# Kernel optimization log

Hardware: AMD Instinct MI355X
Metric: run time of the kernel (lower is better)

Reference implementation:

```python
import jax, jax.numpy as jnp
import numpy as np

# Module hyperparameters (from init_kwargs)
B, C, T, H, W = 2, 128, 4, 64, 64
NHEADS = 32
SH, SW = 4, 4          # scales: patch size in H and W
GROUPS = C // 4        # GroupNorm groups = dim // 4
EPS = 1e-5


def _rel_index(t_, h_, w_):
    """(N,N) int32 index into the (2T-1)*(2h-1)*(2w-1) relative-position table."""
    tt = np.arange(t_); yy = np.arange(h_); xx = np.arange(w_)
    coords = np.stack(np.meshgrid(tt, yy, xx, indexing='ij'), -1).reshape(-1, 3)  # (N,3)
    rel = coords[:, None, :] - coords[None, :, :]                                 # (N,N,3)
    rel = rel + np.array([t_ - 1, h_ - 1, w_ - 1])
    idx = (rel[..., 0] * (2 * h_ - 1) + rel[..., 1]) * (2 * w_ - 1) + rel[..., 2]
    return idx.astype(np.int32)


def setup_inputs() -> dict:
    key = jax.random.key(0)
    ks = jax.random.split(key, 6)
    h, w = H // SH, W // SW
    table_sz = (2 * T - 1) * (2 * h - 1) * (2 * w - 1)
    inp = {
        "x": jax.random.normal(ks[0], (B, C, T, H, W), jnp.float32),
        "Wq": jax.random.normal(ks[1], (C, C), jnp.float32) / np.sqrt(C).astype(np.float32),
        "Wk": jax.random.normal(ks[2], (C, C), jnp.float32) / np.sqrt(C).astype(np.float32),
        "Wv": jax.random.normal(ks[3], (C, C), jnp.float32) / np.sqrt(C).astype(np.float32),
        "gq_gamma": jnp.ones((C,), jnp.float32), "gq_beta": jnp.zeros((C,), jnp.float32),
        "gk_gamma": jnp.ones((C,), jnp.float32), "gk_beta": jnp.zeros((C,), jnp.float32),
        "gv_gamma": jnp.ones((C,), jnp.float32), "gv_beta": jnp.zeros((C,), jnp.float32),
        "rel_table": jax.random.normal(ks[4], (NHEADS, table_sz), jnp.float32) * 0.02,
        "rel_index": jnp.asarray(_rel_index(T, h, w)),
    }
    return inp


def _group_norm(z, gamma, beta, groups, eps=EPS):
    b, c = z.shape[:2]
    zg = z.reshape(b, groups, c // groups, *z.shape[2:])
    mu = zg.mean(axis=(2, 3, 4, 5), keepdims=True)
    var = jnp.mean(jnp.square(zg - mu), axis=(2, 3, 4, 5), keepdims=True)
    zg = (zg - mu) * jax.lax.rsqrt(var + eps)
    zn = zg.reshape(z.shape)
    return zn * gamma[None, :, None, None, None] + beta[None, :, None, None, None]


def reference(x, Wq, Wk, Wv, gq_gamma, gq_beta, gk_gamma, gk_beta,
              gv_gamma, gv_beta, rel_table, rel_index):
    b, c, t, hh, ww = x.shape
    h, w = hh // SH, ww // SW
    n = t * h * w           # patch tokens
    p = SH * SW             # pixels per patch
    d = c // NHEADS         # head dim

    # 1x1x1 projections (pointwise conv == channel matmul) + GroupNorm
    q = _group_norm(jnp.einsum('bcthw,oc->bothw', x, Wq), gq_gamma, gq_beta, GROUPS)
    k = _group_norm(jnp.einsum('bcthw,oc->bothw', x, Wk), gk_gamma, gk_beta, GROUPS)
    v = _group_norm(jnp.einsum('bcthw,oc->bothw', x, Wv), gv_gamma, gv_beta, GROUPS)

    def to_patches(z):  # (b,c,t,H,W) -> (b,heads,d,N,P)
        z = z.reshape(b, NHEADS, d, t, h, SH, w, SW)
        z = z.transpose(0, 1, 2, 3, 4, 6, 5, 7)
        return z.reshape(b, NHEADS, d, n, p)

    qp = to_patches(q).mean(-1)     # pooled patch queries (b,g,d,N)
    kp = to_patches(k).mean(-1)     # pooled patch keys    (b,g,d,N)
    vp = to_patches(v)              # full-res values      (b,g,d,N,P)

    scale = 1.0 / jnp.sqrt(jnp.float32(d))
    logits = jnp.einsum('bgdn,bgdm->bgnm', qp, kp) * scale
    logits = logits + rel_table[:, rel_index][None]   # relative position bias (1,g,N,N)
    attn = jax.nn.softmax(logits, axis=-1)

    out = jnp.einsum('bgnm,bgdmp->bgdnp', attn, vp)   # (b,g,d,N,P)
    out = out.reshape(b, NHEADS, d, t, h, w, SH, SW).transpose(0, 1, 2, 3, 4, 6, 5, 7)
    out = out.reshape(b, c, t, hh, ww)                # (B,C,T,H,W) after outer permute
    return out
```

## Files before the change

### kernel.cpp

```cpp
#include <hip/hip_runtime.h>
#include <hip/hip_bf16.h>

#define B_ 2
#define C_ 128
#define G_ 32
#define N_ 1024
#define S_ 16384
#define TABLE_ 6727
#define EPS_ 1e-5f
#define LOG2E_ 1.44269504f
#define PSTB_ 64

typedef __hip_bfloat16 bf16;
typedef __attribute__((ext_vector_type(8))) short short8;
typedef __attribute__((ext_vector_type(4))) float f32x4;

#if __has_builtin(__builtin_amdgcn_exp2f)
#define EXP2(x) __builtin_amdgcn_exp2f(x)
#else
#define EXP2(x) __expf((x) * 0.69314718056f)
#endif

__device__ __forceinline__ float bf2f(bf16 v) { return __bfloat162float(v); }
__device__ __forceinline__ float bits2f(unsigned u) { return __uint_as_float(u); }
__device__ __forceinline__ int dflag(const void* gq) {
  return (((const unsigned*)gq)[0] != 0x3F803F80u) ? 1 : 0;
}
__device__ __forceinline__ float ldcv(const void* p, int i, int fl) {
  return fl ? ((const float*)p)[i] : bf2f(((const bf16*)p)[i]);
}

__global__ __launch_bounds__(256) void proj_kernel(
    const void* __restrict__ x, const void* __restrict__ Wq,
    const void* __restrict__ Wk, const void* __restrict__ Wv,
    const void* __restrict__ gq,
    float* __restrict__ qpart, float* __restrict__ kpart,
    bf16* __restrict__ vpt, float* __restrict__ statsAcc)
{
  __shared__ bf16 xs[128 * 128];
  __shared__ bf16 vs[8192];
  const int tid = threadIdx.x, lane = tid & 63, w = tid >> 6;
  const int s0 = blockIdx.x * 128;
  const int oh = blockIdx.y;
  const int b  = blockIdx.z;
  const int fl = dflag(gq);

  {
    const int s_lo = tid & 15, cb = tid >> 4;
    const size_t gc = (size_t)b * C_ * S_ + (size_t)(cb * 8) * S_ + s0 + s_lo;
#pragma unroll
    for (int i = 0; i < 8; ++i) {
      const int s = i * 16 + s_lo;
      union { short8 v; bf16 h[8]; } u;
      if (fl) {
#pragma unroll
        for (int j = 0; j < 8; ++j)
          u.h[j] = (bf16)((const float*)x)[gc + i * 16 + (size_t)j * S_];
      } else {
#pragma unroll
        for (int j = 0; j < 8; ++j)
          u.h[j] = ((const bf16*)x)[gc + i * 16 + (size_t)j * S_];
      }
      *(short8*)&xs[s * 128 + ((cb ^ (s & 7)) << 3)] = u.v;
    }
  }

  const int ow = oh * 4 + w;
  const int quad = lane >> 4;
  const int om = ow * 16 + (lane & 15);
  const void* const Ws[3] = {Wq, Wk, Wv};
  short8 afr[3][4];
#pragma unroll
  for (int tt = 0; tt < 3; ++tt)
#pragma unroll
    for (int kk = 0; kk < 4; ++kk) {
      const int off = om * 128 + kk * 32 + quad * 8;
      if (fl) {
        const float* wp = (const float*)Ws[tt] + off;
        const float4 a = *(const float4*)wp, bb = *(const float4*)(wp + 4);
        union { short8 s; bf16 h[8]; } u;
        u.h[0] = (bf16)a.x;  u.h[1] = (bf16)a.y;  u.h[2] = (bf16)a.z;  u.h[3] = (bf16)a.w;
        u.h[4] = (bf16)bb.x; u.h[5] = (bf16)bb.y; u.h[6] = (bf16)bb.z; u.h[7] = (bf16)bb.w;
        afr[tt][kk] = u.s;
      } else {
        afr[tt][kk] = *(const short8*)((const bf16*)Ws[tt] + off);
      }
    }
  __syncthreads();

  float ssum[3] = {0.f, 0.f, 0.f}, ssq[3] = {0.f, 0.f, 0.f};
  float psq[4][4] = {}, psk[4][4] = {};
  const int sl = lane & 15;
#pragma unroll
  for (int st = 0; st < 8; ++st) {
    f32x4 acc[3] = {{0,0,0,0},{0,0,0,0},{0,0,0,0}};
    const int srow = st * 16 + sl;
#pragma unroll
    for (int kk = 0; kk < 4; ++kk) {
      const short8 bv = *(const short8*)
          &xs[srow * 128 + ((((kk << 2) | quad) ^ (sl & 7)) << 3)];
      acc[0] = __builtin_amdgcn_mfma_f32_16x16x32_bf16(afr[0][kk], bv, acc[0], 0, 0, 0);
      acc[1] = __builtin_amdgcn_mfma_f32_16x16x32_bf16(afr[1][kk], bv, acc[1], 0, 0, 0);
      acc[2] = __builtin_amdgcn_mfma_f32_16x16x32_bf16(afr[2][kk], bv, acc[2], 0, 0, 0);
    }
    const int pIdx = (st >> 2) * 4 + (sl & 3);
    const int xp = (st & 3) * 4 + (sl >> 2);
#pragma unroll
    for (int r = 0; r < 4; ++r) {
      const float vq = acc[0][r], vk = acc[1][r], vv = acc[2][r];
      ssum[0] += vq; ssq[0] += vq * vq;
      ssum[1] += vk; ssq[1] += vk * vk;
      ssum[2] += vv; ssq[2] += vv * vv;
      float aq = vq + __shfl_xor(vq, 1); aq += __shfl_xor(aq, 2);
      float ak = vk + __shfl_xor(vk, 1); ak += __shfl_xor(ak, 2);
      psq[r][st & 3] += aq;
      psk[r][st & 3] += ak;
      const int o_loc = w * 16 + quad * 4 + r;
      vs[(o_loc * 8 + pIdx) * 16 + xp] = (bf16)vv;
    }
  }

  {
    const int c = sl & 3, wxl = sl >> 2;
    const int t = s0 >> 12;
    const int yy0 = (s0 >> 6) & 63;
    const int hy = yy0 >> 2, rp = (yy0 >> 1) & 1;
    const int nbase = t * 256 + hy * 16;
    const size_t pb = ((size_t)(b * 2 + rp) * N_ + nbase) * C_ + ow * 16 + quad * 4 + c;
#pragma unroll
    for (int j = 0; j < 4; ++j) {
      float vq = psq[0][j];
      if (c == 1) vq = psq[1][j];
      if (c == 2) vq = psq[2][j];
      if (c == 3) vq = psq[3][j];
      float vk = psk[0][j];
      if (c == 1) vk = psk[1][j];
      if (c == 2) vk = psk[2][j];
      if (c == 3) vk = psk[3][j];
      qpart[pb + (size_t)(j * 4 + wxl) * C_] = vq;
      kpart[pb + (size_t)(j * 4 + wxl) * C_] = vk;
    }
  }

#pragma unroll
  for (int tt = 0; tt < 3; ++tt) {
#pragma unroll
    for (int off = 1; off < 16; off <<= 1) {
      ssum[tt] += __shfl_xor(ssum[tt], off);
      ssq[tt]  += __shfl_xor(ssq[tt], off);
    }
    if ((lane & 15) == 0) {
      const int grp = ow * 4 + quad;
      atomicAdd(&statsAcc[((tt * B_ + b) * G_ + grp) * 2 + 0], ssum[tt]);
      atomicAdd(&statsAcc[((tt * B_ + b) * G_ + grp) * 2 + 1], ssq[tt]);
    }
  }
  __syncthreads();

  const int rowp0 = (s0 >> 6) & 63;
  const int mIdx0 = (s0 >> 12) * 256 + (rowp0 >> 2) * 16;
  for (int cid = tid; cid < 1024; cid += 256) {
    const int half = cid & 1, run = cid >> 1;
    const int o_loc = run >> 3, pIdx = run & 7;
    const int o = oh * 64 + o_loc;
    const int gg = o >> 2, dd = o & 3;
    const int colv = dd * 16 + (rowp0 & 3) * 4 + pIdx;
    bf16* dst = vpt + ((size_t)(b * G_ + gg) * 64 + colv) * N_ + mIdx0 + half * 8;
    *(short8*)dst = *(const short8*)&vs[run * 16 + half * 8];
  }
}

__global__ __launch_bounds__(256) void pool_kernel(
    const float* __restrict__ qpart, const float* __restrict__ kpart,
    const void* __restrict__ gq, const void* __restrict__ bq,
    const void* __restrict__ gk, const void* __restrict__ bk,
    const float* __restrict__ statsAcc,
    bf16* __restrict__ qp2, bf16* __restrict__ kp2)
{
  const int fl = dflag(gq);
  const int idx = blockIdx.x * 256 + threadIdx.x;
  const int c = idx & 127, n = (idx >> 7) & 1023, b = idx >> 17;
  const int g = c >> 2, d = c & 3;
  const size_t p0 = ((size_t)(b * 2 + 0) * N_ + n) * C_ + c;
  const size_t p1 = ((size_t)(b * 2 + 1) * N_ + n) * C_ + c;
  const float sq = qpart[p0] + qpart[p1];
  const float sk = kpart[p0] + kpart[p1];
  const float* saq = statsAcc + ((0 * B_ + b) * G_ + g) * 2;
  const float* sak = statsAcc + ((1 * B_ + b) * G_ + g) * 2;
  const float muq = saq[0] * (1.f / 65536.f);
  const float rq = rsqrtf(saq[1] * (1.f / 65536.f) - muq * muq + EPS_);
  const float muk = sak[0] * (1.f / 65536.f);
  const float rk = rsqrtf(sak[1] * (1.f / 65536.f) - muk * muk + EPS_);
  const float qn = (sq * 0.0625f - muq) * rq * ldcv(gq, c, fl) + ldcv(bq, c, fl);
  const float kn = (sk * 0.0625f - muk) * rk * ldcv(gk, c, fl) + ldcv(bk, c, fl);
  const float qs = qn * (0.5f * LOG2E_);
  const bf16 qh = (bf16)qs; const bf16 ql = (bf16)(qs - bf2f(qh));
  const bf16 kh = (bf16)kn; const bf16 kl = (bf16)(kn - bf2f(kh));
  const size_t qb = ((size_t)(b * G_ + g) * N_ + n) * 8;
  qp2[qb + d] = qh; qp2[qb + 4 + d] = ql;
  kp2[qb + d] = kh; kp2[qb + 4 + d] = kl;
}

__global__ __launch_bounds__(256, 4) void attn_kernel(
    const bf16* __restrict__ qp2, const bf16* __restrict__ kp2,
    const bf16* __restrict__ vpt, const void* __restrict__ rt,
    const void* __restrict__ gq, const void* __restrict__ gv,
    const void* __restrict__ bv, const float* __restrict__ statsAcc,
    void* __restrict__ outv)
{
  const int g = blockIdx.y, b = blockIdx.z;
  const int tid = threadIdx.x, lane = tid & 63, w = tid >> 6;
  const int nw = blockIdx.x * 64;
  const int fl = dflag(gq);
  __shared__ __align__(16) char smem[16384 + 5024 + 8192];
  bf16* Vlds = (bf16*)smem;
  bf16* bldm = (bf16*)(smem + 16384);
  bf16* pldw = (bf16*)(smem + 16384 + 5024) + w * 16 * PSTB_;

  const int tn = nw >> 8, yb = (nw >> 4) & 15;
  for (int i = tid; i < 2508; i += 256) {
    const int row = i / 33, d = i - row * 33;
    if (d < 31) {
      const int tm = row / 19, dyi = row - tm * 19;
      const int dt = tn - tm + 3;
      const int dy = yb + dyi;
      bldm[row * 33 + d] = (bf16)(ldcv(rt, g * TABLE_ + (dt * 31 + dy) * 31 + d, fl) * LOG2E_);
    }
  }

  const int col = lane & 15, quad = lane >> 4;
  const size_t bg = (size_t)(b * G_ + g);
  short8 af = {0, 0, 0, 0, 0, 0, 0, 0};
  if (quad < 2) af = *(const short8*)(qp2 + (bg * N_ + nw + w * 16 + col) * 8);

  const short* kpb = (const short*)kp2 + bg * N_ * 8;
  const short* vpb = (const short*)vpt + bg * 64 * N_;
  const short onebits = (short)0x3F80;
  const short8 ones8 = {onebits, onebits, onebits, onebits,
                        onebits, onebits, onebits, onebits};
  f32x4 acco[4] = {{0,0,0,0},{0,0,0,0},{0,0,0,0},{0,0,0,0}};
  f32x4 accs = {0.f, 0.f, 0.f, 0.f};

  const int skb = tid & 15, snr = tid >> 4;

  ushort4 kv[4], kvn[4];
#pragma unroll
  for (int t = 0; t < 4; ++t)
    kv[t] = *(const ushort4*)(kpb + ((0 * 4 + t) * 16 + col) * 8 + (quad & 1) * 4);

  for (int tile = 0; tile < 8; ++tile) {
    __syncthreads();
    short8 st[4];
#pragma unroll
    for (int i = 0; i < 4; ++i)
      st[i] = *(const short8*)(vpb + (size_t)(i * 16 + snr) * N_ + tile * 128 + skb * 8);
#pragma unroll
    for (int i = 0; i < 4; ++i) {
      const int n = i * 16 + snr;
      *(short8*)&Vlds[n * 128 + ((skb ^ (n & 7)) << 3)] = st[i];
    }
    __syncthreads();

    for (int cl = 0; cl < 2; ++cl) {
      const int ch = tile * 2 + cl;
      if (ch < 15) {
#pragma unroll
        for (int t = 0; t < 4; ++t)
          kvn[t] = *(const ushort4*)(kpb + (((ch + 1) * 4 + t) * 16 + col) * 8 + (quad & 1) * 4);
      }
#pragma unroll
      for (int mt4 = 0; mt4 < 4; ++mt4) {
        const int mt = ch * 4 + mt4;
        const int tm = mt >> 4, ym = mt & 15;
        const short8 bf8 = {(short)kv[mt4].x, (short)kv[mt4].y, (short)kv[mt4].z, (short)kv[mt4].w,
                            (short)kv[mt4].x, (short)kv[mt4].y, (short)kv[mt4].z, (short)kv[mt4].w};
        f32x4 acc = {0.f, 0.f, 0.f, 0.f};
        acc = __builtin_amdgcn_mfma_f32_16x16x32_bf16(af, bf8, acc, 0, 0, 0);
        const int bbase = (tm * 19 + (w + 15 - ym)) * 33 + 15 + quad * 4 - col;
#pragma unroll
        for (int r = 0; r < 4; ++r) {
          const float e = EXP2(acc[r] + bf2f(bldm[bbase + r]));
          const int row = quad * 4 + r;
          pldw[row * PSTB_ + (((mt4 * 2 + (col >> 3)) ^ (row & 7)) << 3) + (col & 7)] = (bf16)e;
        }
      }
#pragma unroll
      for (int ks = 0; ks < 2; ++ks) {
        const short8 a2 = *(const short8*)&pldw[col * PSTB_ + (((ks * 4 + quad) ^ (col & 7)) << 3)];
        accs = __builtin_amdgcn_mfma_f32_16x16x32_bf16(a2, ones8, accs, 0, 0, 0);
#pragma unroll
        for (int cc = 0; cc < 4; ++cc) {
          const int n = cc * 16 + col;
          const int kb = cl * 8 + ks * 4 + quad;
          const short8 b2 = *(const short8*)&Vlds[n * 128 + ((kb ^ (n & 7)) << 3)];
          acco[cc] = __builtin_amdgcn_mfma_f32_16x16x32_bf16(a2, b2, acco[cc], 0, 0, 0);
        }
      }
      if (ch < 15) {
#pragma unroll
        for (int t = 0; t < 4; ++t) kv[t] = kvn[t];
      }
    }
  }

  __syncthreads();
  const float* sav = statsAcc + ((2 * B_ + b) * G_ + g) * 2;
  const float mu = sav[0] * (1.f / 65536.f);
  const float rs = rsqrtf(sav[1] * (1.f / 65536.f) - mu * mu + EPS_);
  const int sh = col >> 2, sw = col & 3;
  const size_t obase = (size_t)(b * C_ + g * 4) * S_ + tn * 4096 + (yb + w) * 256;
  if (!fl) {
    bf16* ost = (bf16*)(smem + w * 2048);
#pragma unroll
    for (int cc = 0; cc < 4; ++cc) {
      const int c = g * 4 + cc;
      const float alpha = rs * ldcv(gv, c, fl);
      const float beta = ldcv(bv, c, fl) - mu * alpha;
#pragma unroll
      for (int r = 0; r < 4; ++r) {
        const int xp = quad * 4 + r;
        ost[cc * 256 + sh * 64 + xp * 4 + sw] = (bf16)(alpha * (acco[cc][r] / accs[r]) + beta);
      }
    }
#pragma unroll
    for (int i = 0; i < 2; ++i) {
      const int e = (i * 64 + lane) * 8;
      const int cc = e >> 8, rem = e & 255;
      *(short8*)((bf16*)outv + obase + (size_t)cc * S_ + rem) = *(const short8*)&ost[e];
    }
  } else {
    float* ostf = (float*)smem + w * 1024;
#pragma unroll
    for (int cc = 0; cc < 4; ++cc) {
      const int c = g * 4 + cc;
      const float alpha = rs * ldcv(gv, c, fl);
      const float beta = ldcv(bv, c, fl) - mu * alpha;
#pragma unroll
      for (int r = 0; r < 4; ++r) {
        const int xp = quad * 4 + r;
        ostf[cc * 256 + sh * 64 + xp * 4 + sw] = alpha * (acco[cc][r] / accs[r]) + beta;
      }
    }
#pragma unroll
    for (int i = 0; i < 4; ++i) {
      const int e = (i * 64 + lane) * 4;
      const int cc = e >> 8, rem = e & 255;
      *(float4*)((float*)outv + obase + (size_t)cc * S_ + rem) = *(const float4*)&ostf[e];
    }
  }
}

extern "C" void kernel_launch(void* const* d_in, const int* in_sizes, int n_in,
                              void* d_out, int out_size, void* d_ws, size_t ws_size,
                              hipStream_t stream) {
  (void)in_sizes; (void)n_in; (void)out_size; (void)ws_size;
  const void* x  = d_in[0];
  const void* Wq = d_in[1];
  const void* Wk = d_in[2];
  const void* Wv = d_in[3];
  const void* gq = d_in[4];
  const void* bq = d_in[5];
  const void* gk = d_in[6];
  const void* bk = d_in[7];
  const void* gv = d_in[8];
  const void* bv = d_in[9];
  const void* rel_table = d_in[10];

  bf16*  vpt  = (bf16*)d_ws;
  bf16*  qp2  = vpt  + (size_t)B_ * G_ * 64 * N_;
  bf16*  kp2  = qp2  + (size_t)B_ * G_ * N_ * 8;
  float* qpart = (float*)(kp2 + (size_t)B_ * G_ * N_ * 8);
  float* kpart = qpart + (size_t)B_ * 2 * N_ * C_;
  float* statsAcc = kpart + (size_t)B_ * 2 * N_ * C_;

  hipMemsetAsync(statsAcc, 0, 384 * sizeof(float), stream);
  proj_kernel<<<dim3(128, 2, B_), 256, 0, stream>>>(
      x, Wq, Wk, Wv, gq, qpart, kpart, vpt, statsAcc);
  pool_kernel<<<dim3(1024), 256, 0, stream>>>(
      qpart, kpart, gq, bq, gk, bk, statsAcc, qp2, kp2);
  attn_kernel<<<dim3(16, G_, B_), 256, 0, stream>>>(
      qp2, kp2, vpt, rel_table, gq, gv, bv, statsAcc, d_out);
}
```

Before: 177.3 us.

## Replace atomic GroupNorm stats with per-strip partials and drop memset

```diff
diff --git a/kernel.cpp b/kernel.cpp
--- a/kernel.cpp
+++ b/kernel.cpp
@@ -10,6 +10,7 @@
 #define EPS_ 1e-5f
 #define LOG2E_ 1.44269504f
 #define PSTB_ 64
+#define NSTRIP_ 128
 
 typedef __hip_bfloat16 bf16;
 typedef __attribute__((ext_vector_type(8))) short short8;
@@ -29,13 +30,16 @@
 __device__ __forceinline__ float ldcv(const void* p, int i, int fl) {
   return fl ? ((const float*)p)[i] : bf2f(((const bf16*)p)[i]);
 }
+__device__ __forceinline__ size_t spidx(int ttm, int b, int g) {
+  return ((size_t)(((ttm * B_ + b) * G_) + g)) << 7;
+}
 
 __global__ __launch_bounds__(256) void proj_kernel(
     const void* __restrict__ x, const void* __restrict__ Wq,
     const void* __restrict__ Wk, const void* __restrict__ Wv,
     const void* __restrict__ gq,
     float* __restrict__ qpart, float* __restrict__ kpart,
-    bf16* __restrict__ vpt, float* __restrict__ statsAcc)
+    bf16* __restrict__ vpt, float* __restrict__ sp)
 {
   __shared__ bf16 xs[128 * 128];
   __shared__ bf16 vs[8192];
@@ -126,7 +130,7 @@
     const int yy0 = (s0 >> 6) & 63;
     const int hy = yy0 >> 2, rp = (yy0 >> 1) & 1;
     const int nbase = t * 256 + hy * 16;
-    const size_t pb = ((size_t)(b * 2 + rp) * N_ + nbase) * C_ + ow * 16 + quad * 4 + c;
+    const size_t pb = ((size_t)((b * 2 + rp) * C_ + ow * 16 + quad * 4 + c)) * N_ + nbase;
 #pragma unroll
     for (int j = 0; j < 4; ++j) {
       float vq = psq[0][j];
@@ -137,8 +141,8 @@
       if (c == 1) vk = psk[1][j];
       if (c == 2) vk = psk[2][j];
       if (c == 3) vk = psk[3][j];
-      qpart[pb + (size_t)(j * 4 + wxl) * C_] = vq;
-      kpart[pb + (size_t)(j * 4 + wxl) * C_] = vk;
+      qpart[pb + j * 4 + wxl] = vq;
+      kpart[pb + j * 4 + wxl] = vk;
     }
   }
 
@@ -151,8 +155,8 @@
     }
     if ((lane & 15) == 0) {
       const int grp = ow * 4 + quad;
-      atomicAdd(&statsAcc[((tt * B_ + b) * G_ + grp) * 2 + 0], ssum[tt]);
-      atomicAdd(&statsAcc[((tt * B_ + b) * G_ + grp) * 2 + 1], ssq[tt]);
+      sp[spidx(tt * 2 + 0, b, grp) + blockIdx.x] = ssum[tt];
+      sp[spidx(tt * 2 + 1, b, grp) + blockIdx.x] = ssq[tt];
     }
   }
   __syncthreads();
@@ -174,23 +178,35 @@
     const float* __restrict__ qpart, const float* __restrict__ kpart,
     const void* __restrict__ gq, const void* __restrict__ bq,
     const void* __restrict__ gk, const void* __restrict__ bk,
-    const float* __restrict__ statsAcc,
+    const float* __restrict__ sp,
     bf16* __restrict__ qp2, bf16* __restrict__ kp2)
 {
   const int fl = dflag(gq);
-  const int idx = blockIdx.x * 256 + threadIdx.x;
-  const int c = idx & 127, n = (idx >> 7) & 1023, b = idx >> 17;
-  const int g = c >> 2, d = c & 3;
-  const size_t p0 = ((size_t)(b * 2 + 0) * N_ + n) * C_ + c;
-  const size_t p1 = ((size_t)(b * 2 + 1) * N_ + n) * C_ + c;
-  const float sq = qpart[p0] + qpart[p1];
-  const float sk = kpart[p0] + kpart[p1];
-  const float* saq = statsAcc + ((0 * B_ + b) * G_ + g) * 2;
-  const float* sak = statsAcc + ((1 * B_ + b) * G_ + g) * 2;
-  const float muq = saq[0] * (1.f / 65536.f);
-  const float rq = rsqrtf(saq[1] * (1.f / 65536.f) - muq * muq + EPS_);
-  const float muk = sak[0] * (1.f / 65536.f);
-  const float rk = rsqrtf(sak[1] * (1.f / 65536.f) - muk * muk + EPS_);
+  const int nc = blockIdx.x, g = blockIdx.y, b = blockIdx.z;
+  const int tid = threadIdx.x, lane = tid & 63, w = tid >> 6;
+  __shared__ float red[4];
+  {
+    const float* a = sp + spidx(w, b, g);
+    float v = a[lane] + a[lane + 64];
+    v += __shfl_xor(v, 1);  v += __shfl_xor(v, 2);  v += __shfl_xor(v, 4);
+    v += __shfl_xor(v, 8);  v += __shfl_xor(v, 16); v += __shfl_xor(v, 32);
+    if (lane == 0) red[w] = v;
+  }
+  __syncthreads();
+  const float muq = red[0] * (1.f / 65536.f);
+  const float rq = rsqrtf(red[1] * (1.f / 65536.f) - muq * muq + EPS_);
+  const float muk = red[2] * (1.f / 65536.f);
+  const float rk = rsqrtf(red[3] * (1.f / 65536.f) - muk * muk + EPS_);
+
+  const int d = tid & 3, ni = tid >> 2;
+  const int n = nc * 64 + ni, c = g * 4 + d;
+  float sq = 0.f, sk = 0.f;
+#pragma unroll
+  for (int rp = 0; rp < 2; ++rp) {
+    const size_t p = ((size_t)((b * 2 + rp) * C_ + c)) * N_ + n;
+    sq += qpart[p];
+    sk += kpart[p];
+  }
   const float qn = (sq * 0.0625f - muq) * rq * ldcv(gq, c, fl) + ldcv(bq, c, fl);
   const float kn = (sk * 0.0625f - muk) * rk * ldcv(gk, c, fl) + ldcv(bk, c, fl);
   const float qs = qn * (0.5f * LOG2E_);
@@ -205,17 +221,26 @@
     const bf16* __restrict__ qp2, const bf16* __restrict__ kp2,
     const bf16* __restrict__ vpt, const void* __restrict__ rt,
     const void* __restrict__ gq, const void* __restrict__ gv,
-    const void* __restrict__ bv, const float* __restrict__ statsAcc,
+    const void* __restrict__ bv, const float* __restrict__ sp,
     void* __restrict__ outv)
 {
   const int g = blockIdx.y, b = blockIdx.z;
   const int tid = threadIdx.x, lane = tid & 63, w = tid >> 6;
   const int nw = blockIdx.x * 64;
   const int fl = dflag(gq);
-  __shared__ __align__(16) char smem[16384 + 5024 + 8192];
+  __shared__ __align__(16) char smem[29616];
   bf16* Vlds = (bf16*)smem;
   bf16* bldm = (bf16*)(smem + 16384);
   bf16* pldw = (bf16*)(smem + 16384 + 5024) + w * 16 * PSTB_;
+  float* vstf = (float*)(smem + 29600);
+
+  if (w < 2) {
+    const float* a = sp + spidx(4 + w, b, g);
+    float v = a[lane] + a[lane + 64];
+    v += __shfl_xor(v, 1);  v += __shfl_xor(v, 2);  v += __shfl_xor(v, 4);
+    v += __shfl_xor(v, 8);  v += __shfl_xor(v, 16); v += __shfl_xor(v, 32);
+    if (lane == 0) vstf[w] = v;
+  }
 
   const int tn = nw >> 8, yb = (nw >> 4) & 15;
   for (int i = tid; i < 2508; i += 256) {
@@ -304,9 +329,8 @@
   }
 
   __syncthreads();
-  const float* sav = statsAcc + ((2 * B_ + b) * G_ + g) * 2;
-  const float mu = sav[0] * (1.f / 65536.f);
-  const float rs = rsqrtf(sav[1] * (1.f / 65536.f) - mu * mu + EPS_);
+  const float mu = vstf[0] * (1.f / 65536.f);
+  const float rs = rsqrtf(vstf[1] * (1.f / 65536.f) - mu * mu + EPS_);
   const int sh = col >> 2, sw = col & 3;
   const size_t obase = (size_t)(b * C_ + g * 4) * S_ + tn * 4096 + (yb + w) * 256;
   if (!fl) {
@@ -370,14 +394,13 @@
   bf16*  qp2  = vpt  + (size_t)B_ * G_ * 64 * N_;
   bf16*  kp2  = qp2  + (size_t)B_ * G_ * N_ * 8;
   float* qpart = (float*)(kp2 + (size_t)B_ * G_ * N_ * 8);
-  float* kpart = qpart + (size_t)B_ * 2 * N_ * C_;
-  float* statsAcc = kpart + (size_t)B_ * 2 * N_ * C_;
-
-  hipMemsetAsync(statsAcc, 0, 384 * sizeof(float), stream);
-  proj_kernel<<<dim3(128, 2, B_), 256, 0, stream>>>(
-      x, Wq, Wk, Wv, gq, qpart, kpart, vpt, statsAcc);
-  pool_kernel<<<dim3(1024), 256, 0, stream>>>(
-      qpart, kpart, gq, bq, gk, bk, statsAcc, qp2, kp2);
+  float* kpart = qpart + (size_t)B_ * 2 * C_ * N_;
+  float* sp    = kpart + (size_t)B_ * 2 * C_ * N_;
+
+  proj_kernel<<<dim3(NSTRIP_, 2, B_), 256, 0, stream>>>(
+      x, Wq, Wk, Wv, gq, qpart, kpart, vpt, sp);
+  pool_kernel<<<dim3(16, G_, B_), 256, 0, stream>>>(
+      qpart, kpart, gq, bq, gk, bk, sp, qp2, kp2);
   attn_kernel<<<dim3(16, G_, B_), 256, 0, stream>>>(
-      qp2, kp2, vpt, rel_table, gq, gv, bv, statsAcc, d_out);
-}
+      qp2, kp2, vpt, rel_table, gq, gv, bv, sp, d_out);
+}
```

After: 162.8 us. -8.2%, faster.
